# Kernel tuning notes

Hardware: AMD Instinct MI355X
Metric: run time of the kernel (lower is better)

Reference implementation:

```python
import jax, jax.numpy as jnp
import numpy as np

B, L, C, H = 1, 2048, 2048, 16
D = C // H
EPS = 1e-6
W0 = 30.0  # SIREN frequency

def rmsnorm(x, w, eps=EPS):
    return x * jax.lax.rsqrt(jnp.mean(x * x, axis=-1, keepdims=True) + eps) * w

def depth_rope(x, depth, base=10000.0):
    # same rotation for all positions, angle set by scalar layer depth
    d = x.shape[-1]
    half = d // 2
    freqs = 1.0 / base ** (jnp.arange(half, dtype=x.dtype) / half)
    ang = depth * freqs
    cos, sin = jnp.cos(ang), jnp.sin(ang)
    x1, x2 = x[..., :half], x[..., half:2 * half]
    return jnp.concatenate([x1 * cos - x2 * sin, x1 * sin + x2 * cos], axis=-1)

def setup_inputs() -> dict:
    key = jax.random.key(0)
    ks = jax.random.split(key, 13)
    s = 1.0 / np.sqrt(C)
    inp = {
        'x':  jax.random.normal(ks[0], (B, L, C), jnp.float32),
        'h0': jax.random.normal(ks[1], (B, L, C), jnp.float32),
        'h1': jax.random.normal(ks[2], (B, L, C), jnp.float32),
        'h2': jax.random.normal(ks[3], (B, L, C), jnp.float32),
        'Wq': jax.random.normal(ks[4], (C, C), jnp.float32) * s,
        'Wk': jax.random.normal(ks[5], (C, C), jnp.float32) * s,
        'Wv': jax.random.normal(ks[6], (C, C), jnp.float32) * s,
        'Wo': jax.random.normal(ks[7], (C, C), jnp.float32) * s,
        'qn_w': jnp.ones((D,), jnp.float32),
        'kn_w': jnp.ones((D,), jnp.float32),
        'on_w': jnp.ones((C,), jnp.float32),
        'sw1': jax.random.normal(ks[8], (1, C), jnp.float32),
        'sb1': jax.random.normal(ks[9], (C,), jnp.float32) * 0.01,
        'sw2': jax.random.normal(ks[10], (C, C), jnp.float32) * s,
        'sb2': jnp.zeros((C,), jnp.float32),
    }
    return inp

def reference(x, h0, h1, h2, Wq, Wk, Wv, Wo, qn_w, kn_w, on_w, sw1, sb1, sw2, sb2):
    history = [h0, h1, h2]
    q_src = history[-1]                      # [B,L,C]
    q_depth = len(history) - 1
    # Q path: proj -> per-head RMSNorm -> depth RoPE
    q = jnp.einsum('blc,oc->blo', q_src, Wq).reshape(B, L, H, D)
    q = depth_rope(rmsnorm(q, qn_w), q_depth)
    # K/V path over prior history entries (each with its own depth)
    k_parts, v_parts = [], []
    for depth_idx, kv in enumerate(history[:-1]):
        k_i = jnp.einsum('blc,oc->blo', kv, Wk).reshape(B, L, H, D)
        v_i = jnp.einsum('blc,oc->blo', kv, Wv).reshape(B, L, H, D)
        k_parts.append(depth_rope(rmsnorm(k_i, kn_w), depth_idx))
        v_parts.append(v_i)
    k = jnp.concatenate(k_parts, axis=1)     # [B,Lkv,H,D]
    v = jnp.concatenate(v_parts, axis=1)
    # full SDPA, default scale D^-0.5
    scores = jnp.einsum('bqhd,bkhd->bhqk', q, k) * (D ** -0.5)
    attn = jax.nn.softmax(scores, axis=-1)
    out = jnp.einsum('bhqk,bkhd->bqhd', attn, v).reshape(B, L, C)
    out = jnp.einsum('blc,oc->blo', out, Wo)
    # SIREN upsample to (L,): target length == L -> identity interpolation
    # plus sine-activated coordinate MLP (implicit positional field)
    coords = jnp.linspace(-1.0, 1.0, L, dtype=x.dtype)[:, None]   # [L,1]
    pos = jnp.sin(W0 * (coords @ sw1 + sb1)) @ sw2 + sb2           # [L,C]
    out = out + pos[None]
    return x + rmsnorm(out, on_w)
```

## Files before the change

kernel.cpp:

```cpp
#include <hip/hip_runtime.h>
#include <hip/hip_fp16.h>

#define LQ 2048
#define CDIM 2048
#define NHEAD 16
#define HDIM 128
#define LKEY 4096

typedef _Float16 f16x8 __attribute__((ext_vector_type(8)));
typedef _Float16 f16x4 __attribute__((ext_vector_type(4)));
typedef float f32x4 __attribute__((ext_vector_type(4)));

#define GLOAD_LDS16(g, s) __builtin_amdgcn_global_load_lds( \
    (const __attribute__((address_space(1))) void*)(g),     \
    (__attribute__((address_space(3))) void*)(s), 16, 0, 0)

#define MFMA16(a, b, c) __builtin_amdgcn_mfma_f32_16x16x32_f16(a, b, c, 0, 0, 0)

__device__ __forceinline__ void storeC(float* p, float v) { *p = v; }
__device__ __forceinline__ void storeC(__half* p, float v) { *p = __float2half(v); }
__device__ __forceinline__ float toF(float v) { return v; }
__device__ __forceinline__ float toF(__half v) { return __half2float(v); }

template <int MODE, typename OutT>
__device__ __forceinline__ void gemm_body(
    __half* smem,
    const __half* __restrict__ A, const __half* __restrict__ B,
    OutT* __restrict__ C, int lda, int ldb, int ldc, int K,
    int bmA, int bmC, int bn,
    const float* __restrict__ wgt, int kmode, float oscale,
    __half* __restrict__ vTo)
{
    __half* lA = smem;
    __half* lB = smem + 8192;
    const int tid  = threadIdx.x;
    const int lane = tid & 63;
    const int wave = tid >> 6;
    const int r = tid >> 3;
    const int g = tid & 7;
    const __half* gA = A + (long)(bmA * 128 + r) * lda + ((g ^ (r & 7)) << 3);
    const __half* gB = B + (long)(bn * 128 + r) * ldb + ((g ^ (r & 7)) << 3);
    __half* lAp = lA + tid * 8;
    __half* lBp = lB + tid * 8;
    const int wr = (wave & 1) << 6;
    const int wc = (wave >> 1) << 6;
    const int l15 = lane & 15, quad = lane >> 4;

    f32x4 acc[4][4] = {};

    for (int kt = 0; kt < K; kt += 64) {
#pragma unroll
        for (int i = 0; i < 4; ++i) {
            GLOAD_LDS16(gA + (long)i * 32 * lda, lAp + i * 2048);
            GLOAD_LDS16(gB + (long)i * 32 * ldb, lBp + i * 2048);
        }
        gA += 64; gB += 64;
        __syncthreads();
#pragma unroll
        for (int kk = 0; kk < 2; ++kk) {
            f16x8 af[4], bfr[4];
#pragma unroll
            for (int mi = 0; mi < 4; ++mi) {
                const int m = wr + mi * 16 + l15;
                const int kg = kk * 4 + quad;
                af[mi] = *(const f16x8*)&lA[m * 64 + ((kg ^ (m & 7)) << 3)];
            }
#pragma unroll
            for (int ni = 0; ni < 4; ++ni) {
                const int n = wc + ni * 16 + l15;
                const int kg = kk * 4 + quad;
                bfr[ni] = *(const f16x8*)&lB[n * 64 + ((kg ^ (n & 7)) << 3)];
            }
#pragma unroll
            for (int mi = 0; mi < 4; ++mi)
#pragma unroll
                for (int ni = 0; ni < 4; ++ni)
                    acc[mi][ni] = MFMA16(af[mi], bfr[ni], acc[mi][ni]);
        }
        __syncthreads();
    }

    if constexpr (MODE == 0) {
        const int row0 = bmC * 128 + wr + quad * 4;
        const int col0 = bn * 128 + wc + l15;
#pragma unroll
        for (int mi = 0; mi < 4; ++mi)
#pragma unroll
            for (int ni = 0; ni < 4; ++ni)
#pragma unroll
                for (int rx = 0; rx < 4; ++rx)
                    storeC(&C[(long)(row0 + mi * 16 + rx) * ldc + col0 + ni * 16],
                           acc[mi][ni][rx]);
    } else if constexpr (MODE == 2) {
#pragma unroll
        for (int mi = 0; mi < 4; ++mi)
#pragma unroll
            for (int ni = 0; ni < 4; ++ni)
#pragma unroll
                for (int rx = 0; rx < 4; ++rx) {
                    const int  d   = (bn - 16) * 128 + wc + ni * 16 + l15;
                    const long key = (long)bmC * 128 + wr + mi * 16 + quad * 4 + rx;
                    vTo[(long)d * LKEY + key] = __float2half(acc[mi][ni][rx]);
                }
    } else {
        __half* sT = smem;
#pragma unroll
        for (int mi = 0; mi < 4; ++mi)
#pragma unroll
            for (int ni = 0; ni < 4; ++ni)
#pragma unroll
                for (int rx = 0; rx < 4; ++rx)
                    sT[(wr + mi * 16 + quad * 4 + rx) * 136 + wc + ni * 16 + l15] =
                        (_Float16)acc[mi][ni][rx];
        __syncthreads();
        const int row = (wave << 5) + (lane >> 1);
        const int c0  = (lane & 1) << 5;
        const __half* rp = sT + row * 136;
        f16x8 L[4], Hh[4];
#pragma unroll
        for (int j8 = 0; j8 < 4; ++j8) {
            L[j8]  = *(const f16x8*)&rp[c0 + j8 * 8];
            Hh[j8] = *(const f16x8*)&rp[c0 + 64 + j8 * 8];
        }
        float ss = 0.f;
#pragma unroll
        for (int j8 = 0; j8 < 4; ++j8)
#pragma unroll
            for (int e = 0; e < 8; ++e) {
                const float a = (float)L[j8][e], b = (float)Hh[j8][e];
                ss += a * a + b * b;
            }
        ss += __shfl_xor(ss, 1);
        const float rn = rsqrtf(ss * (1.0f / 128.0f) + 1e-6f);
        const long grow = (long)bmC * 128 + row;
        const int depth = kmode ? (grow < 2048 ? 0 : 1) : 2;
        union { f16x8 v; _Float16 e[8]; } o1[4], o2[4];
#pragma unroll
        for (int j8 = 0; j8 < 4; ++j8)
#pragma unroll
            for (int e = 0; e < 8; ++e) {
                const int d = c0 + j8 * 8 + e;
                const float x1 = (float)L[j8][e]  * rn * wgt[d];
                const float x2 = (float)Hh[j8][e] * rn * wgt[d + 64];
                const float ang = (float)depth *
                    exp2f(-(float)d * 0.20762050593045702f);
                float sn, cs;
                __sincosf(ang, &sn, &cs);
                o1[j8].e[e] = (_Float16)((x1 * cs - x2 * sn) * oscale);
                o2[j8].e[e] = (_Float16)((x1 * sn + x2 * cs) * oscale);
            }
        __half* op = (__half*)C + grow * ldc + bn * 128;
#pragma unroll
        for (int j8 = 0; j8 < 4; ++j8) {
            *(f16x8*)&op[c0 + j8 * 8]      = o1[j8].v;
            *(f16x8*)&op[c0 + 64 + j8 * 8] = o2[j8].v;
        }
    }
}

__global__ __launch_bounds__(256, 2) void gemm_qkv(
    const __half* __restrict__ A, const __half* __restrict__ Bq,
    const __half* __restrict__ Bkv, __half* __restrict__ Cq,
    __half* __restrict__ Ckv, __half* __restrict__ vT,
    const float* __restrict__ qn_w, const float* __restrict__ kn_w)
{
    __shared__ __align__(16) __half smem[17408];
    const int lin = blockIdx.x;
    if (lin < 1024) {
        const int bm = lin & 31, bn = lin >> 5;
        if (bn < 16)
            gemm_body<1, __half>(smem, A, Bkv, Ckv, 2048, 2048, 4096, 2048,
                                 bm + 16, bm, bn, kn_w, 1, 1.0f, nullptr);
        else
            gemm_body<2, __half>(smem, A, Bkv, Ckv, 2048, 2048, 4096, 2048,
                                 bm + 16, bm, bn, nullptr, 0, 1.0f, vT);
    } else {
        const int l2 = lin - 1024;
        const int bm = l2 & 15, bn = l2 >> 4;
        gemm_body<1, __half>(smem, A, Bq, Cq, 2048, 2048, 2048, 2048,
                             bm, bm, bn, qn_w, 0, 0.12751743f, nullptr);
    }
}

__global__ __launch_bounds__(256, 2) void gemm_sk(
    const __half* __restrict__ A, const __half* __restrict__ B,
    float* __restrict__ C, int lda, int ldb, int ldc, int Kq)
{
    __shared__ __align__(16) __half smem[16384];
    const int z = blockIdx.z;
    gemm_body<0, float>(smem, A + z * Kq, B + z * Kq, C + (long)z * LQ * CDIM,
                        lda, ldb, ldc, Kq, blockIdx.x, blockIdx.x, blockIdx.y,
                        nullptr, 0, 1.0f, nullptr);
}

__global__ __launch_bounds__(256, 2) void attn_tile(
    const __half* __restrict__ Qf,
    const __half* __restrict__ Kf,
    const __half* __restrict__ Vt,
    float* __restrict__ Opart,
    float* __restrict__ lsum)
{
    __shared__ __align__(16) __half lK[64 * 128];
    __shared__ __align__(16) __half lV[128 * 64];
    __shared__ __align__(16) __half pL[4 * 2 * 16 * 76];

    const int tid  = threadIdx.x;
    const int lane = tid & 63;
    const int wave = tid >> 6;
    const int l15  = lane & 15;
    const int quad = lane >> 4;
    const int h  = blockIdx.y >> 1;
    const int kc = blockIdx.y & 1;
    const int q0 = blockIdx.x * 128 + wave * 32;

    f16x8 aq[2][4];
#pragma unroll
    for (int mt = 0; mt < 2; ++mt)
#pragma unroll
        for (int ks = 0; ks < 4; ++ks)
            aq[mt][ks] = *(const f16x8*)&Qf[(long)(q0 + mt * 16 + l15) * CDIM +
                                            h * HDIM + ks * 32 + quad * 8];

    const int rK = tid >> 4;
    const int gK = tid & 15;
    const __half* srcK = Kf + (long)(kc * 2048 + rK) * 4096 + h * HDIM +
                         ((gK ^ (rK & 15)) << 3);
    const int rV = tid >> 3;
    const int gV = tid & 7;
    const __half* srcV = Vt + (long)(h * HDIM + rV) * (long)LKEY + kc * 2048 +
                         ((gV ^ (rV & 7)) << 3);
    __half* dstK = lK + tid * 8;
    __half* dstV = lV + tid * 8;

    f32x4 accO[2][8] = {};
    f32x4 l_acc[2] = {};

    for (int st = 0; st < 32; ++st) {
#pragma unroll
        for (int i = 0; i < 4; ++i) {
            GLOAD_LDS16(srcK + (long)(st * 64 + i * 16) * 4096, dstK + i * 2048);
            GLOAD_LDS16(srcV + (long)i * 32 * LKEY + st * 64, dstV + i * 2048);
        }
        __syncthreads();
        f32x4 s[2][4];
#pragma unroll
        for (int mt = 0; mt < 2; ++mt)
#pragma unroll
            for (int nt = 0; nt < 4; ++nt)
                s[mt][nt] = (f32x4){-10.f, -10.f, -10.f, -10.f};
#pragma unroll
        for (int nt = 0; nt < 4; ++nt) {
            const int n = nt * 16 + l15;
#pragma unroll
            for (int ks = 0; ks < 4; ++ks) {
                const f16x8 kf = *(const f16x8*)
                    &lK[n * 128 + (((ks * 4 + quad) ^ (n & 15)) << 3)];
                s[0][nt] = MFMA16(aq[0][ks], kf, s[0][nt]);
                s[1][nt] = MFMA16(aq[1][ks], kf, s[1][nt]);
            }
        }
#pragma unroll
        for (int mt = 0; mt < 2; ++mt)
#pragma unroll
            for (int nt = 0; nt < 4; ++nt)
#pragma unroll
                for (int r2 = 0; r2 < 4; ++r2) {
                    const float p = __builtin_amdgcn_exp2f(s[mt][nt][r2]);
                    l_acc[mt][r2] += p;
                    pL[((wave * 2 + mt) * 16 + quad * 4 + r2) * 76 +
                       nt * 16 + l15] = __float2half(p);
                }
        f16x8 ap[2][2];
#pragma unroll
        for (int mt = 0; mt < 2; ++mt) {
            ap[mt][0] = *(const f16x8*)&pL[((wave * 2 + mt) * 16 + l15) * 76 + quad * 8];
            ap[mt][1] = *(const f16x8*)&pL[((wave * 2 + mt) * 16 + l15) * 76 + 32 + quad * 8];
        }
#pragma unroll
        for (int nt2 = 0; nt2 < 8; ++nt2) {
            const int n2 = nt2 * 16 + l15;
            const f16x8 v0 = *(const f16x8*)&lV[n2 * 64 + ((quad ^ (n2 & 7)) << 3)];
            const f16x8 v1 = *(const f16x8*)&lV[n2 * 64 + (((4 + quad) ^ (n2 & 7)) << 3)];
            accO[0][nt2] = MFMA16(ap[0][0], v0, accO[0][nt2]);
            accO[0][nt2] = MFMA16(ap[0][1], v1, accO[0][nt2]);
            accO[1][nt2] = MFMA16(ap[1][0], v0, accO[1][nt2]);
            accO[1][nt2] = MFMA16(ap[1][1], v1, accO[1][nt2]);
        }
        __syncthreads();
    }

#pragma unroll
    for (int mt = 0; mt < 2; ++mt)
#pragma unroll
        for (int r2 = 0; r2 < 4; ++r2) {
            float v = l_acc[mt][r2];
            v += __shfl_xor(v, 1);
            v += __shfl_xor(v, 2);
            v += __shfl_xor(v, 4);
            v += __shfl_xor(v, 8);
            if (l15 == 0)
                atomicAdd(&lsum[h * LQ + q0 + mt * 16 + quad * 4 + r2], v);
        }
    float* Cp = Opart + (long)kc * LQ * CDIM + h * HDIM;
#pragma unroll
    for (int mt = 0; mt < 2; ++mt)
#pragma unroll
        for (int nt2 = 0; nt2 < 8; ++nt2)
#pragma unroll
            for (int rx = 0; rx < 4; ++rx)
                Cp[(long)(q0 + mt * 16 + quad * 4 + rx) * CDIM + nt2 * 16 + l15] =
                    accO[mt][nt2][rx];
}

__global__ __launch_bounds__(256) void merge_o(
    const float* __restrict__ Op, const float* __restrict__ lsum,
    __half* __restrict__ a2)
{
    const int row = blockIdx.x;
    const int c0  = threadIdx.x * 8;
    const float inv = 1.0f / lsum[(c0 >> 7) * LQ + row];
    const float* p0 = Op + (long)row * CDIM + c0;
    const float* p1 = p0 + (long)LQ * CDIM;
    union { f16x8 v; _Float16 e[8]; } o;
#pragma unroll
    for (int j = 0; j < 8; ++j)
        o.e[j] = (_Float16)((p0[j] + p1[j]) * inv);
    *(f16x8*)&a2[(long)row * 4096 + c0] = o.v;
}

__global__ __launch_bounds__(256) void cast_all(
    const float* __restrict__ h2, const float* __restrict__ h0,
    const float* __restrict__ h1, const float* __restrict__ Wq,
    const float* __restrict__ Wk, const float* __restrict__ Wv,
    __half* __restrict__ xq, __half* __restrict__ xkv,
    __half* __restrict__ wqh, __half* __restrict__ wkv)
{
    const long i = ((long)blockIdx.x * 256 + threadIdx.x) << 2;
    const int chunk = (int)(i >> 22);
    const long off = i & 4194303;
    const float* s; __half* d;
    switch (chunk) {
        case 0:  s = h2; d = xq;            break;
        case 1:  s = h0; d = xkv;           break;
        case 2:  s = h1; d = xkv + 4194304; break;
        case 3:  s = Wq; d = wqh;           break;
        case 4:  s = Wk; d = wkv;           break;
        default: s = Wv; d = wkv + 4194304; break;
    }
    const float4 v = *(const float4*)&s[off];
    f16x4 o;
    o[0] = (_Float16)v.x; o[1] = (_Float16)v.y;
    o[2] = (_Float16)v.z; o[3] = (_Float16)v.w;
    *(f16x4*)&d[off] = o;
}

__global__ void cast_wo(const float* __restrict__ in, __half* __restrict__ out) {
    const int idx = blockIdx.x * 256 + threadIdx.x;
    const int o = idx >> 11, c = idx & 2047;
    out[((long)o << 12) + c] = __float2half(in[idx]);
}

template <typename InT>
__global__ __launch_bounds__(256) void transpose_h(
    const InT* __restrict__ in, long inStride, long inOff,
    __half* __restrict__ out, long outStride, long outOff)
{
    __shared__ float t[64][65];
    const long r0 = (long)blockIdx.x * 64;
    const long c0 = (long)blockIdx.y * 64;
    const int tj = threadIdx.x & 63;
    const int ti = threadIdx.x >> 6;
#pragma unroll
    for (int it = 0; it < 16; ++it) {
        const int i = it * 4 + ti;
        t[i][tj] = toF(in[(r0 + i) * inStride + inOff + c0 + tj]);
    }
    __syncthreads();
#pragma unroll
    for (int it = 0; it < 16; ++it) {
        const int i = it * 4 + ti;
        out[(c0 + i) * outStride + outOff + r0 + tj] = __float2half(t[tj][i]);
    }
}

__global__ __launch_bounds__(256) void sin_feat(
    const float* __restrict__ sw1, const float* __restrict__ sb1,
    __half* __restrict__ a2)
{
    const int idx = (blockIdx.x * 256 + threadIdx.x) << 2;
    const int l = idx >> 11, c = idx & 2047;
    const float coord = -1.0f + (2.0f / 2047.0f) * (float)l;
    const float4 w = *(const float4*)&sw1[c];
    const float4 b = *(const float4*)&sb1[c];
    f16x4 o;
    o[0] = (_Float16)__sinf(30.0f * (coord * w.x + b.x));
    o[1] = (_Float16)__sinf(30.0f * (coord * w.y + b.y));
    o[2] = (_Float16)__sinf(30.0f * (coord * w.z + b.z));
    o[3] = (_Float16)__sinf(30.0f * (coord * w.w + b.w));
    *(f16x4*)&a2[((long)l << 12) + 2048 + c] = o;
}

__global__ __launch_bounds__(256) void final_norm(
    const float* __restrict__ out2, const float* __restrict__ x,
    const float* __restrict__ sb2, const float* __restrict__ on_w,
    float* __restrict__ y)
{
    const int row = blockIdx.x;
    const float* o0 = out2 + (long)row * CDIM;
    const float* o1 = o0 + 1l * LQ * CDIM;
    const float* o2 = o0 + 2l * LQ * CDIM;
    const float* o3 = o0 + 3l * LQ * CDIM;
    float v[8];
    float ss = 0.f;
#pragma unroll
    for (int i = 0; i < 8; ++i) {
        const int c = threadIdx.x + i * 256;
        const float t = o0[c] + o1[c] + o2[c] + o3[c] + sb2[c];
        v[i] = t;
        ss += t * t;
    }
#pragma unroll
    for (int off = 1; off < 64; off <<= 1) ss += __shfl_xor(ss, off);
    __shared__ float red[4];
    const int lane = threadIdx.x & 63, wv = threadIdx.x >> 6;
    if (lane == 0) red[wv] = ss;
    __syncthreads();
    const float tot = red[0] + red[1] + red[2] + red[3];
    const float rn = rsqrtf(tot * (1.0f / 2048.0f) + 1e-6f);
#pragma unroll
    for (int i = 0; i < 8; ++i) {
        const int c = threadIdx.x + i * 256;
        y[(long)row * CDIM + c] = x[(long)row * CDIM + c] + v[i] * rn * on_w[c];
    }
}

extern "C" void kernel_launch(void* const* d_in, const int* in_sizes, int n_in,
                              void* d_out, int out_size, void* d_ws, size_t ws_size,
                              hipStream_t stream) {
    const float* x    = (const float*)d_in[0];
    const float* h0   = (const float*)d_in[1];
    const float* h1   = (const float*)d_in[2];
    const float* h2   = (const float*)d_in[3];
    const float* Wq   = (const float*)d_in[4];
    const float* Wk   = (const float*)d_in[5];
    const float* Wv   = (const float*)d_in[6];
    const float* Wo   = (const float*)d_in[7];
    const float* qn_w = (const float*)d_in[8];
    const float* kn_w = (const float*)d_in[9];
    const float* on_w = (const float*)d_in[10];
    const float* sw1  = (const float*)d_in[11];
    const float* sb1  = (const float*)d_in[12];
    const float* sw2  = (const float*)d_in[13];
    const float* sb2  = (const float*)d_in[14];
    float* y = (float*)d_out;

    const size_t MB = 1ull << 20;
    char* w = (char*)d_ws;
    __half* xq  = (__half*)(w);
    __half* xkv = (__half*)(w + 8 * MB);
    __half* wqh = (__half*)(w + 24 * MB);
    __half* wkv = (__half*)(w + 32 * MB);
    __half* qf  = (__half*)(w + 48 * MB);
    __half* kvf = (__half*)(w + 56 * MB);
    __half* vT  = (__half*)(w + 88 * MB);
    __half* a2  = (__half*)(w + 104 * MB);
    __half* b2  = (__half*)(w + 120 * MB);
    float* Opart = (float*)(w);
    float* lsum  = (float*)(w + 32 * MB);
    float* out2  = (float*)(w);
    (void)in_sizes; (void)n_in; (void)out_size; (void)ws_size;

    const int n4 = 2048 * 2048;
    cast_all<<<24576, 256, 0, stream>>>(h2, h0, h1, Wq, Wk, Wv, xq, xkv, wqh, wkv);
    cast_wo<<<n4 / 256, 256, 0, stream>>>(Wo, b2);
    transpose_h<float><<<dim3(32, 32), 256, 0, stream>>>(sw2, 2048, 0, b2, 4096, 2048);
    sin_feat<<<4096, 256, 0, stream>>>(sw1, sb1, a2);

    gemm_qkv<<<1280, 256, 0, stream>>>(xq, wqh, wkv, qf, kvf, vT, qn_w, kn_w);

    (void)hipMemsetAsync(lsum, 0, NHEAD * LQ * sizeof(float), stream);
    attn_tile<<<dim3(16, 32), 256, 0, stream>>>(qf, kvf, vT, Opart, lsum);
    merge_o<<<2048, 256, 0, stream>>>(Opart, lsum, a2);

    gemm_sk<<<dim3(16, 16, 4), 256, 0, stream>>>(a2, b2, out2, 4096, 4096, 2048, 1024);
    final_norm<<<2048, 256, 0, stream>>>(out2, x, sb2, on_w, y);
}
```

Baseline: 457.4 us.

## Fuse prep kernels and memset, halve split-K, raise GEMM occupancy bounds

Merges the cast, Wo cast, sw2 transpose, sine-feature and lsum-zeroing launches into one prep kernel, which removes several launches and the memset. The final GEMM now uses split-K of 2 instead of 4, so less fp32 partial output is written and read back, and final_norm is vectorised with float4 and sums only two partials. Both GEMM kernels get launch_bounds min-blocks of 4, which may force register spills in exchange for higher occupancy. lsum moves to its own workspace offset so it no longer overlaps other buffers.

```diff
diff --git a/kernel.cpp b/kernel.cpp
--- a/kernel.cpp
+++ b/kernel.cpp
@@ -19,8 +19,6 @@
 
 __device__ __forceinline__ void storeC(float* p, float v) { *p = v; }
 __device__ __forceinline__ void storeC(__half* p, float v) { *p = __float2half(v); }
-__device__ __forceinline__ float toF(float v) { return v; }
-__device__ __forceinline__ float toF(__half v) { return __half2float(v); }
 
 template <int MODE, typename OutT>
 __device__ __forceinline__ void gemm_body(
@@ -158,7 +156,7 @@
     }
 }
 
-__global__ __launch_bounds__(256, 2) void gemm_qkv(
+__global__ __launch_bounds__(256, 4) void gemm_qkv(
     const __half* __restrict__ A, const __half* __restrict__ Bq,
     const __half* __restrict__ Bkv, __half* __restrict__ Cq,
     __half* __restrict__ Ckv, __half* __restrict__ vT,
@@ -182,14 +180,15 @@
     }
 }
 
-__global__ __launch_bounds__(256, 2) void gemm_sk(
+__global__ __launch_bounds__(256, 4) void gemm_sk(
     const __half* __restrict__ A, const __half* __restrict__ B,
-    float* __restrict__ C, int lda, int ldb, int ldc, int Kq)
+    float* __restrict__ C, int lda, int ldb, int ldc, int Khalf)
 {
     __shared__ __align__(16) __half smem[16384];
     const int z = blockIdx.z;
-    gemm_body<0, float>(smem, A + z * Kq, B + z * Kq, C + (long)z * LQ * CDIM,
-                        lda, ldb, ldc, Kq, blockIdx.x, blockIdx.x, blockIdx.y,
+    gemm_body<0, float>(smem, A + z * Khalf, B + z * Khalf,
+                        C + (long)z * LQ * CDIM,
+                        lda, ldb, ldc, Khalf, blockIdx.x, blockIdx.x, blockIdx.y,
                         nullptr, 0, 1.0f, nullptr);
 }
 
@@ -328,76 +327,79 @@
     *(f16x8*)&a2[(long)row * 4096 + c0] = o.v;
 }
 
-__global__ __launch_bounds__(256) void cast_all(
+__global__ __launch_bounds__(256) void prep_all(
     const float* __restrict__ h2, const float* __restrict__ h0,
     const float* __restrict__ h1, const float* __restrict__ Wq,
     const float* __restrict__ Wk, const float* __restrict__ Wv,
+    const float* __restrict__ Wo, const float* __restrict__ sw1,
+    const float* __restrict__ sb1, const float* __restrict__ sw2,
     __half* __restrict__ xq, __half* __restrict__ xkv,
-    __half* __restrict__ wqh, __half* __restrict__ wkv)
-{
-    const long i = ((long)blockIdx.x * 256 + threadIdx.x) << 2;
-    const int chunk = (int)(i >> 22);
-    const long off = i & 4194303;
-    const float* s; __half* d;
-    switch (chunk) {
-        case 0:  s = h2; d = xq;            break;
-        case 1:  s = h0; d = xkv;           break;
-        case 2:  s = h1; d = xkv + 4194304; break;
-        case 3:  s = Wq; d = wqh;           break;
-        case 4:  s = Wk; d = wkv;           break;
-        default: s = Wv; d = wkv + 4194304; break;
-    }
-    const float4 v = *(const float4*)&s[off];
-    f16x4 o;
-    o[0] = (_Float16)v.x; o[1] = (_Float16)v.y;
-    o[2] = (_Float16)v.z; o[3] = (_Float16)v.w;
-    *(f16x4*)&d[off] = o;
-}
-
-__global__ void cast_wo(const float* __restrict__ in, __half* __restrict__ out) {
-    const int idx = blockIdx.x * 256 + threadIdx.x;
-    const int o = idx >> 11, c = idx & 2047;
-    out[((long)o << 12) + c] = __float2half(in[idx]);
-}
-
-template <typename InT>
-__global__ __launch_bounds__(256) void transpose_h(
-    const InT* __restrict__ in, long inStride, long inOff,
-    __half* __restrict__ out, long outStride, long outOff)
+    __half* __restrict__ wqh, __half* __restrict__ wkv,
+    __half* __restrict__ a2, __half* __restrict__ b2,
+    float* __restrict__ lsum)
 {
     __shared__ float t[64][65];
-    const long r0 = (long)blockIdx.x * 64;
-    const long c0 = (long)blockIdx.y * 64;
-    const int tj = threadIdx.x & 63;
-    const int ti = threadIdx.x >> 6;
-#pragma unroll
-    for (int it = 0; it < 16; ++it) {
-        const int i = it * 4 + ti;
-        t[i][tj] = toF(in[(r0 + i) * inStride + inOff + c0 + tj]);
-    }
-    __syncthreads();
-#pragma unroll
-    for (int it = 0; it < 16; ++it) {
-        const int i = it * 4 + ti;
-        out[(c0 + i) * outStride + outOff + r0 + tj] = __float2half(t[tj][i]);
-    }
-}
-
-__global__ __launch_bounds__(256) void sin_feat(
-    const float* __restrict__ sw1, const float* __restrict__ sb1,
-    __half* __restrict__ a2)
-{
-    const int idx = (blockIdx.x * 256 + threadIdx.x) << 2;
-    const int l = idx >> 11, c = idx & 2047;
-    const float coord = -1.0f + (2.0f / 2047.0f) * (float)l;
-    const float4 w = *(const float4*)&sw1[c];
-    const float4 b = *(const float4*)&sb1[c];
-    f16x4 o;
-    o[0] = (_Float16)__sinf(30.0f * (coord * w.x + b.x));
-    o[1] = (_Float16)__sinf(30.0f * (coord * w.y + b.y));
-    o[2] = (_Float16)__sinf(30.0f * (coord * w.z + b.z));
-    o[3] = (_Float16)__sinf(30.0f * (coord * w.w + b.w));
-    *(f16x4*)&a2[((long)l << 12) + 2048 + c] = o;
+    const int blk = blockIdx.x;
+    const int tid = threadIdx.x;
+    if (blk < 24576) {
+        const long i = ((long)blk * 256 + tid) << 2;
+        const int chunk = (int)(i >> 22);
+        const long off = i & 4194303;
+        const float* s; __half* d;
+        switch (chunk) {
+            case 0:  s = h2; d = xq;            break;
+            case 1:  s = h0; d = xkv;           break;
+            case 2:  s = h1; d = xkv + 4194304; break;
+            case 3:  s = Wq; d = wqh;           break;
+            case 4:  s = Wk; d = wkv;           break;
+            default: s = Wv; d = wkv + 4194304; break;
+        }
+        const float4 v = *(const float4*)&s[off];
+        f16x4 o;
+        o[0] = (_Float16)v.x; o[1] = (_Float16)v.y;
+        o[2] = (_Float16)v.z; o[3] = (_Float16)v.w;
+        *(f16x4*)&d[off] = o;
+    } else if (blk < 28672) {
+        const int i = ((blk - 24576) * 256 + tid) << 2;
+        const int o = i >> 11, c = i & 2047;
+        const float4 v = *(const float4*)&Wo[i];
+        f16x4 w4;
+        w4[0] = (_Float16)v.x; w4[1] = (_Float16)v.y;
+        w4[2] = (_Float16)v.z; w4[3] = (_Float16)v.w;
+        *(f16x4*)&b2[((long)o << 12) + c] = w4;
+    } else if (blk < 29696) {
+        const int lb = blk - 28672;
+        const long r0 = (long)(lb & 31) * 64;
+        const long c0 = (long)(lb >> 5) * 64;
+        const int tj = tid & 63;
+        const int ti = tid >> 6;
+#pragma unroll
+        for (int it = 0; it < 16; ++it) {
+            const int i = it * 4 + ti;
+            t[i][tj] = sw2[(r0 + i) * 2048 + c0 + tj];
+        }
+        __syncthreads();
+#pragma unroll
+        for (int it = 0; it < 16; ++it) {
+            const int i = it * 4 + ti;
+            b2[(c0 + i) * 4096 + 2048 + r0 + tj] = __float2half(t[tj][i]);
+        }
+    } else if (blk < 33792) {
+        const int i = ((blk - 29696) * 256 + tid) << 2;
+        const int l = i >> 11, c = i & 2047;
+        const float coord = -1.0f + (2.0f / 2047.0f) * (float)l;
+        const float4 w = *(const float4*)&sw1[c];
+        const float4 b = *(const float4*)&sb1[c];
+        f16x4 o;
+        o[0] = (_Float16)__sinf(30.0f * (coord * w.x + b.x));
+        o[1] = (_Float16)__sinf(30.0f * (coord * w.y + b.y));
+        o[2] = (_Float16)__sinf(30.0f * (coord * w.z + b.z));
+        o[3] = (_Float16)__sinf(30.0f * (coord * w.w + b.w));
+        *(f16x4*)&a2[((long)l << 12) + 2048 + c] = o;
+    } else {
+        const int i = ((blk - 33792) * 256 + tid) << 2;
+        *(float4*)&lsum[i] = (float4){0.f, 0.f, 0.f, 0.f};
+    }
 }
 
 __global__ __launch_bounds__(256) void final_norm(
@@ -407,17 +409,20 @@
 {
     const int row = blockIdx.x;
     const float* o0 = out2 + (long)row * CDIM;
-    const float* o1 = o0 + 1l * LQ * CDIM;
-    const float* o2 = o0 + 2l * LQ * CDIM;
-    const float* o3 = o0 + 3l * LQ * CDIM;
-    float v[8];
+    const float* o1 = o0 + (long)LQ * CDIM;
+    float4 v[2];
     float ss = 0.f;
 #pragma unroll
-    for (int i = 0; i < 8; ++i) {
-        const int c = threadIdx.x + i * 256;
-        const float t = o0[c] + o1[c] + o2[c] + o3[c] + sb2[c];
-        v[i] = t;
-        ss += t * t;
+    for (int i = 0; i < 2; ++i) {
+        const int c = threadIdx.x * 4 + i * 1024;
+        const float4 a = *(const float4*)&o0[c];
+        const float4 b = *(const float4*)&o1[c];
+        const float4 s = *(const float4*)&sb2[c];
+        float4 tv;
+        tv.x = a.x + b.x + s.x; tv.y = a.y + b.y + s.y;
+        tv.z = a.z + b.z + s.z; tv.w = a.w + b.w + s.w;
+        v[i] = tv;
+        ss += tv.x * tv.x + tv.y * tv.y + tv.z * tv.z + tv.w * tv.w;
     }
 #pragma unroll
     for (int off = 1; off < 64; off <<= 1) ss += __shfl_xor(ss, off);
@@ -428,9 +433,16 @@
     const float tot = red[0] + red[1] + red[2] + red[3];
     const float rn = rsqrtf(tot * (1.0f / 2048.0f) + 1e-6f);
 #pragma unroll
-    for (int i = 0; i < 8; ++i) {
-        const int c = threadIdx.x + i * 256;
-        y[(long)row * CDIM + c] = x[(long)row * CDIM + c] + v[i] * rn * on_w[c];
+    for (int i = 0; i < 2; ++i) {
+        const int c = threadIdx.x * 4 + i * 1024;
+        const float4 xr = *(const float4*)&x[(long)row * CDIM + c];
+        const float4 wv4 = *(const float4*)&on_w[c];
+        float4 o;
+        o.x = xr.x + v[i].x * rn * wv4.x;
+        o.y = xr.y + v[i].y * rn * wv4.y;
+        o.z = xr.z + v[i].z * rn * wv4.z;
+        o.w = xr.w + v[i].w * rn * wv4.w;
+        *(float4*)&y[(long)row * CDIM + c] = o;
     }
 }
 
@@ -465,23 +477,19 @@
     __half* vT  = (__half*)(w + 88 * MB);
     __half* a2  = (__half*)(w + 104 * MB);
     __half* b2  = (__half*)(w + 120 * MB);
+    float* lsum  = (float*)(w + 136 * MB);
     float* Opart = (float*)(w);
-    float* lsum  = (float*)(w + 32 * MB);
     float* out2  = (float*)(w);
     (void)in_sizes; (void)n_in; (void)out_size; (void)ws_size;
 
-    const int n4 = 2048 * 2048;
-    cast_all<<<24576, 256, 0, stream>>>(h2, h0, h1, Wq, Wk, Wv, xq, xkv, wqh, wkv);
-    cast_wo<<<n4 / 256, 256, 0, stream>>>(Wo, b2);
-    transpose_h<float><<<dim3(32, 32), 256, 0, stream>>>(sw2, 2048, 0, b2, 4096, 2048);
-    sin_feat<<<4096, 256, 0, stream>>>(sw1, sb1, a2);
+    prep_all<<<33824, 256, 0, stream>>>(h2, h0, h1, Wq, Wk, Wv, Wo, sw1, sb1,
+                                        sw2, xq, xkv, wqh, wkv, a2, b2, lsum);
 
     gemm_qkv<<<1280, 256, 0, stream>>>(xq, wqh, wkv, qf, kvf, vT, qn_w, kn_w);
 
-    (void)hipMemsetAsync(lsum, 0, NHEAD * LQ * sizeof(float), stream);
     attn_tile<<<dim3(16, 32), 256, 0, stream>>>(qf, kvf, vT, Opart, lsum);
     merge_o<<<2048, 256, 0, stream>>>(Opart, lsum, a2);
 
-    gemm_sk<<<dim3(16, 16, 4), 256, 0, stream>>>(a2, b2, out2, 4096, 4096, 2048, 1024);
+    gemm_sk<<<dim3(16, 16, 2), 256, 0, stream>>>(a2, b2, out2, 4096, 4096, 2048, 2048);
     final_norm<<<2048, 256, 0, stream>>>(out2, x, sb2, on_w, y);
 }
```

Result: slower. 466.9 us (+2.1%).
